# Kernel optimization log

Measured on AMD Instinct MI355X. Metric: run time of the kernel, lower is better.

The kernel has to match this reference:

```python
import jax, jax.numpy as jnp
import numpy as np

B, Q, S, D, H = 4, 1024, 4096, 256, 8
HD = D // H
NEG = -1000000000.0


def setup_inputs() -> dict:
    key = jax.random.key(0)
    ks = jax.random.split(key, 12)
    s = 1.0 / np.sqrt(D)
    inp = {
        "query": jax.random.normal(ks[0], (B, Q, D), jnp.float32),
        "key": jax.random.normal(ks[1], (B, S, D), jnp.float32),
        "value": jax.random.normal(ks[2], (B, S, D), jnp.float32),
        "attention_mask": jax.random.randint(ks[3], (B, Q, S), 0, 2) > 0,
        # nn.Linear weights stored as [out, in]; we apply x @ W.T + b
        "wq": jax.random.uniform(ks[4], (D, D), jnp.float32, -s, s),
        "bq": jnp.zeros((D,), jnp.float32),
        "wk": jax.random.uniform(ks[5], (D, D), jnp.float32, -s, s),
        "bk": jnp.zeros((D,), jnp.float32),
        "wv": jax.random.uniform(ks[6], (D, D), jnp.float32, -s, s),
        "bv": jnp.zeros((D,), jnp.float32),
        "wo": jax.random.uniform(ks[7], (D, D), jnp.float32, -s, s),
        "bo": jnp.zeros((D,), jnp.float32),
        "ln_g": jnp.ones((D,), jnp.float32),
        "ln_b": jnp.zeros((D,), jnp.float32),
    }
    return inp


def _layernorm(x, g, b, eps=1e-5):
    mu = jnp.mean(x, axis=-1, keepdims=True)
    var = jnp.var(x, axis=-1, keepdims=True)
    return (x - mu) * jax.lax.rsqrt(var + eps) * g + b


def reference(query, key, value, attention_mask, wq, bq, wk, bk, wv, bv, wo, bo, ln_g, ln_b):
    residual = query
    x = _layernorm(query, ln_g, ln_b)
    q = x @ wq.T + bq                       # [B,Q,D]
    k = key @ wk.T + bk                     # [B,S,D]
    v = value @ wv.T + bv                   # [B,S,D]
    q = q.reshape(B, Q, H, HD).transpose(0, 2, 1, 3)   # [B,H,Q,HD]
    k = k.reshape(B, S, H, HD).transpose(0, 2, 1, 3)   # [B,H,S,HD]
    v = v.reshape(B, S, H, HD).transpose(0, 2, 1, 3)   # [B,H,S,HD]
    scale = HD ** -0.5
    scores = jnp.einsum("bhqd,bhsd->bhqs", q, k) * scale   # [B,H,Q,S]
    scores = jnp.where(attention_mask[:, None, :, :], scores, NEG)
    attn = jax.nn.softmax(scores, axis=-1)
    # dropout is identity in eval/inference mode
    out = jnp.einsum("bhqs,bhsd->bhqd", attn, v)            # [B,H,Q,HD]
    out = out.transpose(0, 2, 1, 3).reshape(B, Q, D)
    out = out @ wo.T + bo
    return out + residual
```

## Files before the change

kernel.cpp:

```cpp
#include <hip/hip_runtime.h>
#include <cmath>

#define BQ 4
#define QL 1024
#define SL 4096
#define DM 256
#define NH 8
#define HD 32
#define NROWS 32768
#define NSPLIT 4
#define SEG (SL / NSPLIT)

typedef __attribute__((ext_vector_type(8))) short short8;
typedef __attribute__((ext_vector_type(4))) short short4v;
typedef __attribute__((ext_vector_type(4))) float f32x4;
typedef __attribute__((ext_vector_type(4))) unsigned int uint4v;
typedef __attribute__((ext_vector_type(2))) unsigned int uint2v;
typedef unsigned long long u64;

#define MFMA16(a, b, c) __builtin_amdgcn_mfma_f32_16x16x32_bf16((a), (b), (c), 0, 0, 0)

__device__ __forceinline__ short f2bf(float f) {
  union { float f; unsigned int u; } x; x.f = f;
  unsigned int r = x.u + 0x7FFFu + ((x.u >> 16) & 1u);
  return (short)(r >> 16);
}
__device__ __forceinline__ unsigned int fu(float f) {
  union { float f; unsigned int u; } x; x.f = f; return x.u;
}
__device__ __forceinline__ unsigned int cvtpk(float lo, float hi) {
  unsigned int r;
  asm("v_cvt_pk_bf16_f32 %0, %1, %2" : "=v"(r) : "v"(lo), "v"(hi));
  return r;
}

__global__ void detect_kernel(const uint4v* __restrict__ m,
                              unsigned int* __restrict__ flags) {
  __shared__ int fA, fB;
  if (threadIdx.x == 0) { fA = 0; fB = 0; }
  __syncthreads();
  uint4v v = m[threadIdx.x];
  unsigned int a = 0, bb = 0;
#pragma unroll
  for (int e = 0; e < 4; ++e) {
    a |= (v[e] & 0xFEFEFEFEu);
    bb |= (v[e] & 0xFFFFFF00u);
  }
  if (a) atomicOr(&fA, 1);
  if (bb) atomicOr(&fB, 1);
  __syncthreads();
  if (threadIdx.x == 0) flags[0] = (fA || !fB) ? 4u : 1u;
}

__global__ __launch_bounds__(256) void prep_kernel(const float* __restrict__ wq,
                                                   const float* __restrict__ wk,
                                                   const float* __restrict__ wv,
                                                   const float* __restrict__ wo,
                                                   const void* __restrict__ mask,
                                                   const unsigned int* __restrict__ flags,
                                                   short* __restrict__ w16,
                                                   u64* __restrict__ MB,
                                                   const float* __restrict__ x,
                                                   const float* __restrict__ gw,
                                                   const float* __restrict__ bw,
                                                   short* __restrict__ xout) {
  const int bid = blockIdx.x;
  if (bid < 128) {
    const int i = bid * 256 + threadIdx.x;
    const float* src;
    short* dst;
    if (i < 8192)       { src = wq + i * 8;            dst = w16 + i * 8; }
    else if (i < 16384) { src = wk + (i - 8192) * 8;   dst = w16 + 65536 + (i - 8192) * 8; }
    else if (i < 24576) { src = wv + (i - 16384) * 8;  dst = w16 + 131072 + (i - 16384) * 8; }
    else                { src = wo + (i - 24576) * 8;  dst = w16 + 196608 + (i - 24576) * 8; }
    f32x4 a0 = *(const f32x4*)src;
    f32x4 a1 = *(const f32x4*)(src + 4);
    uint4v o = {cvtpk(a0[0], a0[1]), cvtpk(a0[2], a0[3]),
                cvtpk(a1[0], a1[1]), cvtpk(a1[2], a1[3])};
    *(uint4v*)dst = o;
    return;
  }
  const int b2 = bid - 128;
  const int i = b2 * 256 + threadIdx.x;
  u64 bits = 0;
  if (flags[0] == 4u) {
    const uint4v* src = (const uint4v*)mask + (size_t)i * 16;
#pragma unroll
    for (int c = 0; c < 16; ++c) {
      uint4v v = src[c];
      unsigned int nib = 0;
#pragma unroll
      for (int e = 0; e < 4; ++e) nib |= (v[e] != 0u ? 1u : 0u) << e;
      bits |= (u64)nib << ((c & 3) * 16 + (c >> 2) * 4);
    }
  } else {
    const uint4v* src = (const uint4v*)mask + (size_t)i * 4;
#pragma unroll
    for (int c = 0; c < 4; ++c) {
      uint4v v = src[c];
#pragma unroll
      for (int e4 = 0; e4 < 4; ++e4) {
        const unsigned int u = v[e4];
        unsigned int nib = 0;
        nib |= (u & 0x000000FFu) ? 1u : 0u;
        nib |= (u & 0x0000FF00u) ? 2u : 0u;
        nib |= (u & 0x00FF0000u) ? 4u : 0u;
        nib |= (u & 0xFF000000u) ? 8u : 0u;
        bits |= (u64)nib << (e4 * 16 + c * 4);
      }
    }
  }
  MB[i] = bits;
  const int lane = threadIdx.x & 63;
  const int row = b2 * 4 + (threadIdx.x >> 6);
  const float* xr = x + (size_t)row * DM;
  f32x4 v = *(const f32x4*)(xr + lane * 4);
  float s = v[0] + v[1] + v[2] + v[3];
  float s2 = v[0]*v[0] + v[1]*v[1] + v[2]*v[2] + v[3]*v[3];
#pragma unroll
  for (int m = 1; m < 64; m <<= 1) { s += __shfl_xor(s, m); s2 += __shfl_xor(s2, m); }
  const float mu = s * (1.0f / DM);
  const float var = s2 * (1.0f / DM) - mu * mu;
  const float inv = rsqrtf(var + 1e-5f);
  f32x4 gv = *(const f32x4*)(gw + lane * 4);
  f32x4 bv = *(const f32x4*)(bw + lane * 4);
  float y0 = (v[0] - mu) * inv * gv[0] + bv[0];
  float y1 = (v[1] - mu) * inv * gv[1] + bv[1];
  float y2 = (v[2] - mu) * inv * gv[2] + bv[2];
  float y3 = (v[3] - mu) * inv * gv[3] + bv[3];
  uint2v o = {cvtpk(y0, y1), cvtpk(y2, y3)};
  *(uint2v*)(xout + (size_t)row * DM + lane * 4) = o;
}

__global__ __launch_bounds__(256) void proj_kernel(const short* __restrict__ xln,
                                                   const float* __restrict__ key,
                                                   const float* __restrict__ value,
                                                   const short* __restrict__ w16,
                                                   const float* __restrict__ bq,
                                                   const float* __restrict__ bk,
                                                   const float* __restrict__ bv,
                                                   short* __restrict__ qb,
                                                   short* __restrict__ kb,
                                                   short* __restrict__ vbT,
                                                   float qscale) {
  __shared__ __align__(16) short As[2][64][72];
  __shared__ __align__(16) short Bs[2][64][72];
  const int bid = blockIdx.x;
  const int t = threadIdx.x;
  const int lane = t & 63, w = t >> 6;
  const int wm = w >> 1, wn = w & 1;
  const int g = lane >> 4, lr = lane & 15, gsh = g * 4;

  if (bid < 1024) {
    const int x = bid & 7, j = bid >> 3;
    const int m0 = (x * 16 + (j >> 3)) * 32;
    const int n0 = (j & 7) * 32;
    const int row = t >> 3, cc = t & 7;
    const int trow = m0 + row;
    const short* W16 = w16;
    f32x4 acc = {0.f, 0.f, 0.f, 0.f};
    short8 aval = *(const short8*)(xln + (size_t)trow * DM + cc * 8);
    short8 bval = *(const short8*)(W16 + (size_t)(n0 + row) * DM + cc * 8);
    for (int k0 = 0; k0 < 4; ++k0) {
      const int buf = k0 & 1;
      *(short8*)&As[buf][row][cc * 8] = aval;
      *(short8*)&Bs[buf][row][cc * 8] = bval;
      __syncthreads();
      if (k0 < 3) {
        aval = *(const short8*)(xln + (size_t)trow * DM + (k0 + 1) * 64 + cc * 8);
        bval = *(const short8*)(W16 + (size_t)(n0 + row) * DM + (k0 + 1) * 64 + cc * 8);
      }
#pragma unroll
      for (int ks = 0; ks < 2; ++ks) {
        short8 af = *(const short8*)&As[buf][wm * 16 + lr][ks * 32 + g * 8];
        short8 bf = *(const short8*)&Bs[buf][wn * 16 + lr][ks * 32 + g * 8];
        acc = MFMA16(af, bf, acc);
      }
    }
    const int nl = wn * 16 + lr;
    const float bvv = bq[n0 + nl];
#pragma unroll
    for (int r = 0; r < 4; ++r)
      As[0][wm * 16 + gsh + r][nl] = f2bf((acc[r] + bvv) * qscale);
    __syncthreads();
    *(short4v*)(qb + (size_t)trow * DM + n0 + (t & 7) * 4) =
        *(const short4v*)&As[0][row][(t & 7) * 4];
    return;
  }

  const bool isK = (bid < 2048);
  const int bid2 = bid - (isK ? 1024 : 2048);
  const float* Af = isK ? key : value;
  const short* W16 = w16 + (isK ? 65536 : 131072);
  const float* bias = isK ? bk : bv;
  const int x = bid2 & 7, j = bid2 >> 3;
  const int m0 = (x * 32 + (j >> 2)) * 64;
  const int n0 = (j & 3) * 64;
  const int row = (t * 2) >> 3, cc0 = (t * 2) & 7;
  f32x4 acc[2][2] = {};

  f32x4 apf[2][2];
  short8 bn[2];
#pragma unroll
  for (int c = 0; c < 2; ++c) {
    const float* s = Af + (size_t)(m0 + row) * DM + (cc0 + c) * 8;
    apf[c][0] = *(const f32x4*)s;
    apf[c][1] = *(const f32x4*)(s + 4);
    bn[c] = *(const short8*)(W16 + (size_t)(n0 + row) * DM + (cc0 + c) * 8);
  }
  for (int k0 = 0; k0 < 4; ++k0) {
    const int buf = k0 & 1;
#pragma unroll
    for (int c = 0; c < 2; ++c) {
      uint4v sv = {cvtpk(apf[c][0][0], apf[c][0][1]), cvtpk(apf[c][0][2], apf[c][0][3]),
                   cvtpk(apf[c][1][0], apf[c][1][1]), cvtpk(apf[c][1][2], apf[c][1][3])};
      *(uint4v*)&As[buf][row][(cc0 + c) * 8] = sv;
      *(short8*)&Bs[buf][row][(cc0 + c) * 8] = bn[c];
    }
    __syncthreads();
    if (k0 < 3) {
#pragma unroll
      for (int c = 0; c < 2; ++c) {
        const float* s = Af + (size_t)(m0 + row) * DM + (k0 + 1) * 64 + (cc0 + c) * 8;
        apf[c][0] = *(const f32x4*)s;
        apf[c][1] = *(const f32x4*)(s + 4);
        bn[c] = *(const short8*)(W16 + (size_t)(n0 + row) * DM + (k0 + 1) * 64 + (cc0 + c) * 8);
      }
    }
#pragma unroll
    for (int ks = 0; ks < 2; ++ks) {
      short8 af[2], bfr[2];
#pragma unroll
      for (int i = 0; i < 2; ++i) af[i] = *(const short8*)&As[buf][wm * 32 + i * 16 + lr][ks * 32 + g * 8];
#pragma unroll
      for (int jj = 0; jj < 2; ++jj) bfr[jj] = *(const short8*)&Bs[buf][wn * 32 + jj * 16 + lr][ks * 32 + g * 8];
#pragma unroll
      for (int i = 0; i < 2; ++i)
#pragma unroll
        for (int jj = 0; jj < 2; ++jj) acc[i][jj] = MFMA16(af[i], bfr[jj], acc[i][jj]);
    }
  }
  if (isK) {
#pragma unroll
    for (int i = 0; i < 2; ++i)
#pragma unroll
      for (int jj = 0; jj < 2; ++jj) {
        const int nl = wn * 32 + jj * 16 + lr;
        const float bvv = bias[n0 + nl];
#pragma unroll
        for (int r = 0; r < 4; ++r)
          As[0][wm * 32 + i * 16 + gsh + r][nl] = f2bf(acc[i][jj][r] + bvv);
      }
    __syncthreads();
#pragma unroll
    for (int c = 0; c < 2; ++c) {
      const int idx = t * 2 + c, dl = idx >> 3, ch = idx & 7;
      *(short8*)(kb + (size_t)(m0 + dl) * DM + n0 + ch * 8) =
          *(const short8*)&As[0][dl][ch * 8];
    }
  } else {
#pragma unroll
    for (int i = 0; i < 2; ++i)
#pragma unroll
      for (int jj = 0; jj < 2; ++jj) {
        const int nl = wn * 32 + jj * 16 + lr;
        const float bvv = bias[n0 + nl];
        uint2v pk2 = {cvtpk(acc[i][jj][0] + bvv, acc[i][jj][1] + bvv),
                      cvtpk(acc[i][jj][2] + bvv, acc[i][jj][3] + bvv)};
        *(uint2v*)&As[0][nl][wm * 32 + i * 16 + gsh] = pk2;
      }
    __syncthreads();
    const int bidx = m0 >> 12, sbase = m0 & (SL - 1);
#pragma unroll
    for (int c = 0; c < 2; ++c) {
      const int idx = t * 2 + c, dl = idx >> 3, ch = idx & 7;
      *(short8*)(vbT + ((size_t)bidx * DM + n0 + dl) * SL + sbase + ch * 8) =
          *(const short8*)&As[0][dl][ch * 8];
    }
  }
}

__global__ __launch_bounds__(256) void outproj_kernel(const float* __restrict__ Op,
                                                      const float* __restrict__ Lp,
                                                      const short* __restrict__ W16,
                                                      const float* __restrict__ bias,
                                                      float* __restrict__ outp,
                                                      const float* __restrict__ resid) {
  __shared__ __align__(16) short As[2][32][72];
  __shared__ __align__(16) short Bs[2][32][72];
  const int t = threadIdx.x;
  const int lane = t & 63, w = t >> 6;
  const int wm = w >> 1, wn = w & 1;
  const int g = lane >> 4, lr = lane & 15, gsh = g * 4;
  const int bid = blockIdx.x;
  const int x = bid & 7, j = bid >> 3;
  const int m0 = (x * 16 + (j >> 3)) * 32;
  const int n0 = (j & 7) * 32;
  const int row = t >> 3, cc = t & 7;
  const int trow = m0 + row;
  f32x4 acc = {0.f, 0.f, 0.f, 0.f};

  auto produceA = [&](int k) -> short8 {
    const int kcol = k * 64 + cc * 8;
    const int h = kcol >> 5, hd = kcol & 31;
    const size_t rid = ((size_t)((trow >> 10) * NH + h)) * QL + (trow & (QL - 1));
    float den = 0.0f;
    f32x4 o0 = {0.f, 0.f, 0.f, 0.f}, o1 = {0.f, 0.f, 0.f, 0.f};
#pragma unroll
    for (int i = 0; i < NSPLIT; ++i) {
      const size_t base = ((size_t)i * NROWS + rid) * 32 + hd;
      den += Lp[(size_t)i * NROWS + rid];
      const f32x4 pa = *(const f32x4*)(Op + base);
      const f32x4 pb = *(const f32x4*)(Op + base + 4);
#pragma unroll
      for (int e = 0; e < 4; ++e) { o0[e] += pa[e]; o1[e] += pb[e]; }
    }
    const float inv = __builtin_amdgcn_rcpf(den);
    union { uint4v u; short8 s; } pk;
    pk.u = uint4v{cvtpk(o0[0] * inv, o0[1] * inv), cvtpk(o0[2] * inv, o0[3] * inv),
                  cvtpk(o1[0] * inv, o1[1] * inv), cvtpk(o1[2] * inv, o1[3] * inv)};
    return pk.s;
  };
  short8 aval = produceA(0);
  short8 bval = *(const short8*)(W16 + (size_t)(n0 + row) * DM + cc * 8);

  for (int k0 = 0; k0 < 4; ++k0) {
    const int buf = k0 & 1;
    *(short8*)&As[buf][row][cc * 8] = aval;
    *(short8*)&Bs[buf][row][cc * 8] = bval;
    __syncthreads();
    if (k0 < 3) {
      aval = produceA(k0 + 1);
      bval = *(const short8*)(W16 + (size_t)(n0 + row) * DM + (k0 + 1) * 64 + cc * 8);
    }
#pragma unroll
    for (int ks = 0; ks < 2; ++ks) {
      short8 af = *(const short8*)&As[buf][wm * 16 + lr][ks * 32 + g * 8];
      short8 bf = *(const short8*)&Bs[buf][wn * 16 + lr][ks * 32 + g * 8];
      acc = MFMA16(af, bf, acc);
    }
  }
#pragma unroll
  for (int r = 0; r < 4; ++r) {
    const int rr = m0 + wm * 16 + gsh + r;
    const int col = n0 + wn * 16 + lr;
    outp[(size_t)rr * DM + col] = acc[r] + bias[col] + resid[(size_t)rr * DM + col];
  }
}

__global__ __launch_bounds__(256, 4) void attn_kernel(const short* __restrict__ qb,
                                                      const short* __restrict__ kb,
                                                      const short* __restrict__ vbT,
                                                      const unsigned short* __restrict__ MB,
                                                      float* __restrict__ Op,
                                                      float* __restrict__ Lp) {
  __shared__ __align__(16) short Ks[2][64][40];
  __shared__ __align__(16) short Vs[2][32][76];

  const int n_ = blockIdx.x;
  const int x_ = n_ & 7, j_ = n_ >> 3;
  const int grp = ((j_ >> 5) << 3) + x_;
  const int within = j_ & 31;
  const int q0 = (within & 7) * 128;
  const int split = within >> 3;
  const int h = grp & 7, b = grp >> 3;

  const int t = threadIdx.x;
  const int l = t & 63, w = t >> 6;
  const int g = l >> 4, lr = l & 15, gsh = g * 4;
  const int qbase = q0 + w * 32;
  const int srow = t >> 2, scc = t & 3;
  const int vd = t >> 3, vsc = t & 7;

  const short* Kp = kb + ((size_t)b * SL + split * SEG + srow) * DM + h * HD + scc * 8;
  const short* Vp = vbT + ((size_t)(b * NH + h) * HD + vd) * SL + split * SEG + vsc * 8;
  const unsigned short* MBp0 =
      MB + (((size_t)(b * QL) + qbase + lr) * 64 + split * (SEG / 64)) * 4 + g;
  const unsigned short* MBp1 = MBp0 + 16 * 64 * 4;

  const short8 qf0 =
      *(const short8*)(qb + ((size_t)(b * QL) + qbase + lr) * DM + h * HD + g * 8);
  const short8 qf1 =
      *(const short8*)(qb + ((size_t)(b * QL) + qbase + 16 + lr) * DM + h * HD + g * 8);

  const short ONE = (short)0x3F80;
  const short8 ONES = {ONE, ONE, ONE, ONE, ONE, ONE, ONE, ONE};
  f32x4 Ov0[2] = {}, Ov1[2] = {};
  f32x4 Ls0 = {0.f, 0.f, 0.f, 0.f}, Ls1 = {0.f, 0.f, 0.f, 0.f};

  short8 kreg[2], vreg[2];
  unsigned int mbA[2], mbB[2];
  kreg[0] = *(const short8*)Kp;
  vreg[0] = *(const short8*)Vp;
  mbA[0] = MBp0[0]; mbB[0] = MBp1[0];
  kreg[1] = *(const short8*)(Kp + (size_t)64 * DM);
  vreg[1] = *(const short8*)(Vp + 64);
  mbA[1] = MBp0[4]; mbB[1] = MBp1[4];

#pragma unroll 2
  for (int it = 0; it < SEG / 64; ++it) {
    const int buf = it & 1;
    *(short8*)&Ks[buf][srow][scc * 8] = kreg[buf];
    {
      short4v lo = {vreg[buf][0], vreg[buf][1], vreg[buf][2], vreg[buf][3]};
      short4v hi = {vreg[buf][4], vreg[buf][5], vreg[buf][6], vreg[buf][7]};
      *(short4v*)&Vs[buf][vd][vsc * 8] = lo;
      *(short4v*)&Vs[buf][vd][vsc * 8 + 4] = hi;
    }
    const unsigned int mb0 = mbA[buf], mb1 = mbB[buf];
    __syncthreads();
    if (it < SEG / 64 - 2) {
      kreg[buf] = *(const short8*)(Kp + (size_t)(it + 2) * 64 * DM);
      vreg[buf] = *(const short8*)(Vp + (it + 2) * 64);
      mbA[buf] = MBp0[(it + 2) * 4];
      mbB[buf] = MBp1[(it + 2) * 4];
    }

    const f32x4 z = {0.f, 0.f, 0.f, 0.f};
    f32x4 sc0[4], sc1[4];
    __builtin_amdgcn_s_setprio(1);
#pragma unroll
    for (int f = 0; f < 4; ++f) {
      short8 kf = *(const short8*)&Ks[buf][f * 16 + lr][g * 8];
      sc0[f] = MFMA16(kf, qf0, z);
      sc1[f] = MFMA16(kf, qf1, z);
    }
    __builtin_amdgcn_s_setprio(0);
#pragma unroll
    for (int ks = 0; ks < 2; ++ks) {
      unsigned int pk0[2][2], pk1[2][2];
#pragma unroll
      for (int fi = 0; fi < 2; ++fi) {
        const int f = 2 * ks + fi;
        unsigned int p0[4], p1[4];
#pragma unroll
        for (int r = 0; r < 4; ++r) {
          const int sh = 31 - (f * 4 + r);
          const unsigned int m0b = (unsigned int)(((int)(mb0 << sh)) >> 31);
          const unsigned int m1b = (unsigned int)(((int)(mb1 << sh)) >> 31);
          p0[r] = fu(__builtin_amdgcn_exp2f(sc0[f][r])) & m0b;
          p1[r] = fu(__builtin_amdgcn_exp2f(sc1[f][r])) & m1b;
        }
        pk0[fi][0] = __builtin_amdgcn_perm(p0[0], p0[1], 0x03020706u);
        pk0[fi][1] = __builtin_amdgcn_perm(p0[2], p0[3], 0x03020706u);
        pk1[fi][0] = __builtin_amdgcn_perm(p1[0], p1[1], 0x03020706u);
        pk1[fi][1] = __builtin_amdgcn_perm(p1[2], p1[3], 0x03020706u);
      }
      union { unsigned int u[4]; short8 v; } pa0, pa1;
      pa0.u[0] = pk0[0][0]; pa0.u[1] = pk0[0][1]; pa0.u[2] = pk0[1][0]; pa0.u[3] = pk0[1][1];
      pa1.u[0] = pk1[0][0]; pa1.u[1] = pk1[0][1]; pa1.u[2] = pk1[1][0]; pa1.u[3] = pk1[1][1];
      __builtin_amdgcn_s_setprio(1);
      Ls0 = MFMA16(pa0.v, ONES, Ls0);
      Ls1 = MFMA16(pa1.v, ONES, Ls1);
#pragma unroll
      for (int n = 0; n < 2; ++n) {
        short4v va = *(const short4v*)&Vs[buf][n * 16 + lr][(2 * ks) * 16 + gsh];
        short4v vb2 = *(const short4v*)&Vs[buf][n * 16 + lr][(2 * ks + 1) * 16 + gsh];
        union { short4v h[2]; short8 v; } vf;
        vf.h[0] = va; vf.h[1] = vb2;
        Ov0[n] = MFMA16(pa0.v, vf.v, Ov0[n]);
        Ov1[n] = MFMA16(pa1.v, vf.v, Ov1[n]);
      }
      __builtin_amdgcn_s_setprio(0);
    }
  }
  const int ridx = (b * NH + h) * QL + qbase;
  const size_t pb = (size_t)split * NROWS + ridx;
#pragma unroll
  for (int n = 0; n < 2; ++n)
#pragma unroll
    for (int r = 0; r < 4; ++r) {
      Op[(pb + gsh + r) * 32 + n * 16 + lr] = Ov0[n][r];
      Op[(pb + 16 + gsh + r) * 32 + n * 16 + lr] = Ov1[n][r];
    }
  if (lr == 0) {
#pragma unroll
    for (int r = 0; r < 4; ++r) {
      Lp[pb + gsh + r] = Ls0[r];
      Lp[pb + 16 + gsh + r] = Ls1[r];
    }
  }
}

extern "C" void kernel_launch(void* const* d_in, const int* in_sizes, int n_in,
                              void* d_out, int out_size, void* d_ws, size_t ws_size,
                              hipStream_t stream) {
  const float* query = (const float*)d_in[0];
  const float* key   = (const float*)d_in[1];
  const float* value = (const float*)d_in[2];
  const void*  mask  = d_in[3];
  const float* wq = (const float*)d_in[4];
  const float* bq = (const float*)d_in[5];
  const float* wk = (const float*)d_in[6];
  const float* bk = (const float*)d_in[7];
  const float* wv = (const float*)d_in[8];
  const float* bv = (const float*)d_in[9];
  const float* wo = (const float*)d_in[10];
  const float* bo = (const float*)d_in[11];
  const float* lng = (const float*)d_in[12];
  const float* lnb = (const float*)d_in[13];
  float* out = (float*)d_out;

  char* ws = (char*)d_ws;
  unsigned int* flags = (unsigned int*)ws;
  float* Lp  = (float*)(ws + (4u << 10));
  short* xln = (short*)(ws + (2u << 20));
  short* qb  = (short*)(ws + (4u << 20));
  short* kb  = (short*)(ws + (6u << 20));
  short* vbT = (short*)(ws + (14u << 20));
  u64*   mbt = (u64*)(ws + (22u << 20));
  short* w16 = (short*)(ws + (24u << 20));
  float* Op  = (float*)(ws + (25u << 20));

  const float qscale = (float)(1.4426950408889634 / sqrt((double)HD));

  detect_kernel<<<1, 256, 0, stream>>>((const uint4v*)mask, flags);
  prep_kernel<<<1152, 256, 0, stream>>>(wq, wk, wv, wo, mask, flags, w16, mbt,
                                        query, lng, lnb, xln);
  proj_kernel<<<3072, 256, 0, stream>>>(xln, key, value, w16, bq, bk, bv,
                                        qb, kb, vbT, qscale);
  attn_kernel<<<1024, 256, 0, stream>>>(qb, kb, vbT, (const unsigned short*)mbt, Op, Lp);
  outproj_kernel<<<1024, 256, 0, stream>>>(Op, Lp, w16 + 196608, bo, out, query);
}
```

Baseline: 87.86 us.

## Fold mask-format detection into prep kernel and load full K in projection

Removes the separate single-block detect kernel launch by having each mask-packing block in prep_kernel redundantly compute the mask format flag in shared memory. The projection kernel drops its double-buffered 4-step K loop and instead loads the whole 256-wide K slice into a larger shared tile in one shot, then runs all MFMAs after a single barrier. This cuts launch overhead and per-iteration barriers but raises shared memory use (about 66 KB per block) and register pressure, which may reduce occupancy and remove load/compute overlap.

```diff
diff --git a/kernel.cpp b/kernel.cpp
--- a/kernel.cpp
+++ b/kernel.cpp
@@ -34,30 +34,11 @@
   return r;
 }
 
-__global__ void detect_kernel(const uint4v* __restrict__ m,
-                              unsigned int* __restrict__ flags) {
-  __shared__ int fA, fB;
-  if (threadIdx.x == 0) { fA = 0; fB = 0; }
-  __syncthreads();
-  uint4v v = m[threadIdx.x];
-  unsigned int a = 0, bb = 0;
-#pragma unroll
-  for (int e = 0; e < 4; ++e) {
-    a |= (v[e] & 0xFEFEFEFEu);
-    bb |= (v[e] & 0xFFFFFF00u);
-  }
-  if (a) atomicOr(&fA, 1);
-  if (bb) atomicOr(&fB, 1);
-  __syncthreads();
-  if (threadIdx.x == 0) flags[0] = (fA || !fB) ? 4u : 1u;
-}
-
 __global__ __launch_bounds__(256) void prep_kernel(const float* __restrict__ wq,
                                                    const float* __restrict__ wk,
                                                    const float* __restrict__ wv,
                                                    const float* __restrict__ wo,
                                                    const void* __restrict__ mask,
-                                                   const unsigned int* __restrict__ flags,
                                                    short* __restrict__ w16,
                                                    u64* __restrict__ MB,
                                                    const float* __restrict__ x,
@@ -81,9 +62,25 @@
     return;
   }
   const int b2 = bid - 128;
+  __shared__ int fA, fB;
+  if (threadIdx.x == 0) { fA = 0; fB = 0; }
+  __syncthreads();
+  {
+    uint4v v = ((const uint4v*)mask)[threadIdx.x];
+    unsigned int a = 0, bb2 = 0;
+#pragma unroll
+    for (int e = 0; e < 4; ++e) {
+      a |= (v[e] & 0xFEFEFEFEu);
+      bb2 |= (v[e] & 0xFFFFFF00u);
+    }
+    if (a) atomicOr(&fA, 1);
+    if (bb2) atomicOr(&fB, 1);
+  }
+  __syncthreads();
+  const bool mode4 = (fA || !fB);
   const int i = b2 * 256 + threadIdx.x;
   u64 bits = 0;
-  if (flags[0] == 4u) {
+  if (mode4) {
     const uint4v* src = (const uint4v*)mask + (size_t)i * 16;
 #pragma unroll
     for (int c = 0; c < 16; ++c) {
@@ -143,8 +140,8 @@
                                                    short* __restrict__ kb,
                                                    short* __restrict__ vbT,
                                                    float qscale) {
-  __shared__ __align__(16) short As[2][64][72];
-  __shared__ __align__(16) short Bs[2][64][72];
+  __shared__ __align__(16) short As[64][264];
+  __shared__ __align__(16) short Bs[64][264];
   const int bid = blockIdx.x;
   const int t = threadIdx.x;
   const int lane = t & 63, w = t >> 6;
@@ -155,36 +152,36 @@
     const int x = bid & 7, j = bid >> 3;
     const int m0 = (x * 16 + (j >> 3)) * 32;
     const int n0 = (j & 7) * 32;
-    const int row = t >> 3, cc = t & 7;
+    const int row = t >> 3, cb = (t & 7) * 32;
     const int trow = m0 + row;
-    const short* W16 = w16;
+    short8 a4[4], b4[4];
+#pragma unroll
+    for (int jj = 0; jj < 4; ++jj) {
+      a4[jj] = *(const short8*)(xln + (size_t)trow * DM + cb + jj * 8);
+      b4[jj] = *(const short8*)(w16 + (size_t)(n0 + row) * DM + cb + jj * 8);
+    }
+#pragma unroll
+    for (int jj = 0; jj < 4; ++jj) {
+      *(short8*)&As[row][cb + jj * 8] = a4[jj];
+      *(short8*)&Bs[row][cb + jj * 8] = b4[jj];
+    }
+    __syncthreads();
     f32x4 acc = {0.f, 0.f, 0.f, 0.f};
-    short8 aval = *(const short8*)(xln + (size_t)trow * DM + cc * 8);
-    short8 bval = *(const short8*)(W16 + (size_t)(n0 + row) * DM + cc * 8);
-    for (int k0 = 0; k0 < 4; ++k0) {
-      const int buf = k0 & 1;
-      *(short8*)&As[buf][row][cc * 8] = aval;
-      *(short8*)&Bs[buf][row][cc * 8] = bval;
-      __syncthreads();
-      if (k0 < 3) {
-        aval = *(const short8*)(xln + (size_t)trow * DM + (k0 + 1) * 64 + cc * 8);
-        bval = *(const short8*)(W16 + (size_t)(n0 + row) * DM + (k0 + 1) * 64 + cc * 8);
-      }
-#pragma unroll
-      for (int ks = 0; ks < 2; ++ks) {
-        short8 af = *(const short8*)&As[buf][wm * 16 + lr][ks * 32 + g * 8];
-        short8 bf = *(const short8*)&Bs[buf][wn * 16 + lr][ks * 32 + g * 8];
-        acc = MFMA16(af, bf, acc);
-      }
-    }
+#pragma unroll
+    for (int kk = 0; kk < 8; ++kk) {
+      short8 af = *(const short8*)&As[wm * 16 + lr][kk * 32 + g * 8];
+      short8 bf = *(const short8*)&Bs[wn * 16 + lr][kk * 32 + g * 8];
+      acc = MFMA16(af, bf, acc);
+    }
+    __syncthreads();
     const int nl = wn * 16 + lr;
     const float bvv = bq[n0 + nl];
 #pragma unroll
     for (int r = 0; r < 4; ++r)
-      As[0][wm * 16 + gsh + r][nl] = f2bf((acc[r] + bvv) * qscale);
+      As[wm * 16 + gsh + r][nl] = f2bf((acc[r] + bvv) * qscale);
     __syncthreads();
     *(short4v*)(qb + (size_t)trow * DM + n0 + (t & 7) * 4) =
-        *(const short4v*)&As[0][row][(t & 7) * 4];
+        *(const short4v*)&As[row][(t & 7) * 4];
     return;
   }
 
@@ -196,50 +193,39 @@
   const int x = bid2 & 7, j = bid2 >> 3;
   const int m0 = (x * 32 + (j >> 2)) * 64;
   const int n0 = (j & 3) * 64;
-  const int row = (t * 2) >> 3, cc0 = (t * 2) & 7;
+  const int r = t >> 2, cb = (t & 3) * 64;
+
+  f32x4 av[16];
+  short8 bv8[8];
+#pragma unroll
+  for (int jj = 0; jj < 16; ++jj)
+    av[jj] = *(const f32x4*)(Af + (size_t)(m0 + r) * DM + cb + jj * 4);
+#pragma unroll
+  for (int jj = 0; jj < 8; ++jj)
+    bv8[jj] = *(const short8*)(W16 + (size_t)(n0 + r) * DM + cb + jj * 8);
+#pragma unroll
+  for (int jj = 0; jj < 8; ++jj) {
+    uint4v sv = {cvtpk(av[2 * jj][0], av[2 * jj][1]), cvtpk(av[2 * jj][2], av[2 * jj][3]),
+                 cvtpk(av[2 * jj + 1][0], av[2 * jj + 1][1]),
+                 cvtpk(av[2 * jj + 1][2], av[2 * jj + 1][3])};
+    *(uint4v*)&As[r][cb + jj * 8] = sv;
+    *(short8*)&Bs[r][cb + jj * 8] = bv8[jj];
+  }
+  __syncthreads();
   f32x4 acc[2][2] = {};
-
-  f32x4 apf[2][2];
-  short8 bn[2];
-#pragma unroll
-  for (int c = 0; c < 2; ++c) {
-    const float* s = Af + (size_t)(m0 + row) * DM + (cc0 + c) * 8;
-    apf[c][0] = *(const f32x4*)s;
-    apf[c][1] = *(const f32x4*)(s + 4);
-    bn[c] = *(const short8*)(W16 + (size_t)(n0 + row) * DM + (cc0 + c) * 8);
-  }
-  for (int k0 = 0; k0 < 4; ++k0) {
-    const int buf = k0 & 1;
-#pragma unroll
-    for (int c = 0; c < 2; ++c) {
-      uint4v sv = {cvtpk(apf[c][0][0], apf[c][0][1]), cvtpk(apf[c][0][2], apf[c][0][3]),
-                   cvtpk(apf[c][1][0], apf[c][1][1]), cvtpk(apf[c][1][2], apf[c][1][3])};
-      *(uint4v*)&As[buf][row][(cc0 + c) * 8] = sv;
-      *(short8*)&Bs[buf][row][(cc0 + c) * 8] = bn[c];
-    }
-    __syncthreads();
-    if (k0 < 3) {
-#pragma unroll
-      for (int c = 0; c < 2; ++c) {
-        const float* s = Af + (size_t)(m0 + row) * DM + (k0 + 1) * 64 + (cc0 + c) * 8;
-        apf[c][0] = *(const f32x4*)s;
-        apf[c][1] = *(const f32x4*)(s + 4);
-        bn[c] = *(const short8*)(W16 + (size_t)(n0 + row) * DM + (k0 + 1) * 64 + (cc0 + c) * 8);
-      }
-    }
-#pragma unroll
-    for (int ks = 0; ks < 2; ++ks) {
-      short8 af[2], bfr[2];
-#pragma unroll
-      for (int i = 0; i < 2; ++i) af[i] = *(const short8*)&As[buf][wm * 32 + i * 16 + lr][ks * 32 + g * 8];
-#pragma unroll
-      for (int jj = 0; jj < 2; ++jj) bfr[jj] = *(const short8*)&Bs[buf][wn * 32 + jj * 16 + lr][ks * 32 + g * 8];
-#pragma unroll
-      for (int i = 0; i < 2; ++i)
-#pragma unroll
-        for (int jj = 0; jj < 2; ++jj) acc[i][jj] = MFMA16(af[i], bfr[jj], acc[i][jj]);
-    }
-  }
+#pragma unroll
+  for (int kk = 0; kk < 8; ++kk) {
+    short8 af[2], bfr[2];
+#pragma unroll
+    for (int i = 0; i < 2; ++i) af[i] = *(const short8*)&As[wm * 32 + i * 16 + lr][kk * 32 + g * 8];
+#pragma unroll
+    for (int jj = 0; jj < 2; ++jj) bfr[jj] = *(const short8*)&Bs[wn * 32 + jj * 16 + lr][kk * 32 + g * 8];
+#pragma unroll
+    for (int i = 0; i < 2; ++i)
+#pragma unroll
+      for (int jj = 0; jj < 2; ++jj) acc[i][jj] = MFMA16(af[i], bfr[jj], acc[i][jj]);
+  }
+  __syncthreads();
   if (isK) {
 #pragma unroll
     for (int i = 0; i < 2; ++i)
@@ -248,15 +234,15 @@
         const int nl = wn * 32 + jj * 16 + lr;
         const float bvv = bias[n0 + nl];
 #pragma unroll
-        for (int r = 0; r < 4; ++r)
-          As[0][wm * 32 + i * 16 + gsh + r][nl] = f2bf(acc[i][jj][r] + bvv);
+        for (int rr = 0; rr < 4; ++rr)
+          As[wm * 32 + i * 16 + gsh + rr][nl] = f2bf(acc[i][jj][rr] + bvv);
       }
     __syncthreads();
 #pragma unroll
     for (int c = 0; c < 2; ++c) {
       const int idx = t * 2 + c, dl = idx >> 3, ch = idx & 7;
       *(short8*)(kb + (size_t)(m0 + dl) * DM + n0 + ch * 8) =
-          *(const short8*)&As[0][dl][ch * 8];
+          *(const short8*)&As[dl][ch * 8];
     }
   } else {
 #pragma unroll
@@ -267,7 +253,7 @@
         const float bvv = bias[n0 + nl];
         uint2v pk2 = {cvtpk(acc[i][jj][0] + bvv, acc[i][jj][1] + bvv),
                       cvtpk(acc[i][jj][2] + bvv, acc[i][jj][3] + bvv)};
-        *(uint2v*)&As[0][nl][wm * 32 + i * 16 + gsh] = pk2;
+        *(uint2v*)&As[nl][wm * 32 + i * 16 + gsh] = pk2;
       }
     __syncthreads();
     const int bidx = m0 >> 12, sbase = m0 & (SL - 1);
@@ -275,7 +261,7 @@
     for (int c = 0; c < 2; ++c) {
       const int idx = t * 2 + c, dl = idx >> 3, ch = idx & 7;
       *(short8*)(vbT + ((size_t)bidx * DM + n0 + dl) * SL + sbase + ch * 8) =
-          *(const short8*)&As[0][dl][ch * 8];
+          *(const short8*)&As[dl][ch * 8];
     }
   }
 }
@@ -502,7 +488,6 @@
   float* out = (float*)d_out;
 
   char* ws = (char*)d_ws;
-  unsigned int* flags = (unsigned int*)ws;
   float* Lp  = (float*)(ws + (4u << 10));
   short* xln = (short*)(ws + (2u << 20));
   short* qb  = (short*)(ws + (4u << 20));
@@ -514,8 +499,7 @@
 
   const float qscale = (float)(1.4426950408889634 / sqrt((double)HD));
 
-  detect_kernel<<<1, 256, 0, stream>>>((const uint4v*)mask, flags);
-  prep_kernel<<<1152, 256, 0, stream>>>(wq, wk, wv, wo, mask, flags, w16, mbt,
+  prep_kernel<<<1152, 256, 0, stream>>>(wq, wk, wv, wo, mask, w16, mbt,
                                         query, lng, lnb, xln);
   proj_kernel<<<3072, 256, 0, stream>>>(xln, key, value, w16, bq, bk, bv,
                                         qb, kb, vbT, qscale);
```

Result: slower. 95.83 us (+9.1%).
